# Kernel optimization log

Hardware: AMD Instinct MI355X
Metric: run time of the kernel (lower is better)

The kernel has to match this reference:

```python
import jax, jax.numpy as jnp
import numpy as np

B, T, D_MODEL = 2, 2048, 1024
EXPAND, D_STATE, D_CONV = 2, 16, 4
D_INNER = EXPAND * D_MODEL          # 2048
DT_RANK = (D_MODEL + 15) // 16      # 64 (mamba default: ceil(d_model/16))


def setup_inputs() -> dict:
    key = jax.random.key(0)
    ks = jax.random.split(key, 8)
    g = lambda k, shape, s: jax.random.normal(k, shape, dtype=jnp.float32) * s
    x = jax.random.normal(ks[0], (B, T, D_MODEL), dtype=jnp.float32)
    W_in = g(ks[1], (D_MODEL, 2 * D_INNER), 0.02)
    conv_w = g(ks[2], (D_INNER, D_CONV), 0.1)
    conv_b = jnp.zeros((D_INNER,), jnp.float32)
    W_xproj = g(ks[3], (D_INNER, DT_RANK + 2 * D_STATE), 0.02)
    W_dt = g(ks[4], (DT_RANK, D_INNER), 0.1)
    # dt bias so softplus(b_dt) ~ Uniform[1e-3, 0.1] (mamba init)
    dt = jnp.exp(jax.random.uniform(ks[5], (D_INNER,), jnp.float32)
                 * (np.log(0.1) - np.log(1e-3)) + np.log(1e-3))
    b_dt = dt + jnp.log(-jnp.expm1(-dt))  # inverse softplus
    # A_log init: log(1..d_state) broadcast over channels (S4D-real init)
    A_log = jnp.log(jnp.broadcast_to(
        jnp.arange(1, D_STATE + 1, dtype=jnp.float32), (D_INNER, D_STATE)))
    D = jnp.ones((D_INNER,), jnp.float32)
    W_out = g(ks[6], (D_INNER, D_MODEL), 0.02)
    return dict(x=x, W_in=W_in, conv_w=conv_w, conv_b=conv_b, W_xproj=W_xproj,
                W_dt=W_dt, b_dt=b_dt, A_log=A_log, D=D, W_out=W_out)


def _mamba(x, W_in, conv_w, conv_b, W_xproj, W_dt, b_dt, A_log, D, W_out):
    Bsz, Tlen, _ = x.shape
    xz = x @ W_in                                    # (B,T,2*d_inner)
    u, z = jnp.split(xz, 2, axis=-1)                 # each (B,T,d_inner)
    # causal depthwise conv1d (kernel D_CONV, left-padded)
    up = jnp.pad(u, ((0, 0), (D_CONV - 1, 0), (0, 0)))
    uc = conv_b + sum(up[:, k:k + Tlen, :] * conv_w[:, k] for k in range(D_CONV))
    uc = jax.nn.silu(uc)
    proj = uc @ W_xproj                              # (B,T,dt_rank+2N)
    dt, Bm, Cm = jnp.split(proj, [DT_RANK, DT_RANK + D_STATE], axis=-1)
    delta = jax.nn.softplus(dt @ W_dt + b_dt)        # (B,T,d_inner)
    A = -jnp.exp(A_log)                              # (d_inner,N)
    dA = jnp.exp(delta[..., None] * A)               # (B,T,d_inner,N)
    dBu = delta[..., None] * Bm[:, :, None, :] * uc[..., None]

    def step(h, inp):
        dA_t, dBu_t, C_t = inp                       # (B,d,N),(B,d,N),(B,N)
        h = dA_t * h + dBu_t
        y = jnp.einsum('bdn,bn->bd', h, C_t)
        return h, y

    h0 = jnp.zeros((Bsz, D_INNER, D_STATE), x.dtype)
    _, ys = jax.lax.scan(step, h0, (dA.transpose(1, 0, 2, 3),
                                    dBu.transpose(1, 0, 2, 3),
                                    Cm.transpose(1, 0, 2)))
    y = ys.transpose(1, 0, 2) + uc * D               # (B,T,d_inner)
    y = y * jax.nn.silu(z)                           # gate
    return y @ W_out                                 # (B,T,d_model)


def reference(x, W_in, conv_w, conv_b, W_xproj, W_dt, b_dt, A_log, D, W_out):
    return _mamba(x, W_in, conv_w, conv_b, W_xproj, W_dt, b_dt, A_log, D, W_out)
```

## Files before the change

kernel.cpp:

```cpp
#include <hip/hip_runtime.h>


#define NCHUNK 64
#define CLEN 32

typedef __attribute__((ext_vector_type(8))) short bf16x8;
typedef __attribute__((ext_vector_type(4))) float f32x4;

__device__ __forceinline__ float bf2f(ushort u) {
  union { unsigned u; float f; } x; x.u = ((unsigned)u) << 16; return x.f;
}
__device__ __forceinline__ ushort f2bf(float f) {
  union { float f; unsigned u; } x; x.f = f;
  unsigned r = x.u + 0x7FFFu + ((x.u >> 16) & 1u);
  return (ushort)(r >> 16);
}
__device__ __forceinline__ float siluf(float x) { return x / (1.f + __expf(-x)); }

__device__ __forceinline__ void pow_chain(float g, float* dA) {
  float e2 = g * g;
  float e4 = e2 * e2;
  float e8 = e4 * e4;
  dA[0] = g;        dA[1] = e2;       dA[2] = e2 * g;    dA[3] = e4;
  dA[4] = e4 * g;   dA[5] = e4 * e2;  dA[6] = e4 * dA[2]; dA[7] = e8;
  dA[8] = e8 * g;   dA[9] = e8 * e2;  dA[10] = e8 * dA[2]; dA[11] = e8 * e4;
  dA[12] = e8 * dA[4]; dA[13] = e8 * dA[5]; dA[14] = e8 * dA[6]; dA[15] = e8 * e8;
}

__device__ __forceinline__ void gl_lds16(const ushort* g, ushort* l) {
  __builtin_amdgcn_global_load_lds(
      (const __attribute__((address_space(1))) unsigned*)(size_t)g,
      (__attribute__((address_space(3))) unsigned*)(unsigned)(size_t)l,
      16, 0, 0);
}

__device__ __forceinline__ void phase_barrier() {
  __builtin_amdgcn_sched_barrier(0);
  __builtin_amdgcn_s_barrier();
  __builtin_amdgcn_sched_barrier(0);
}
#define VM8() asm volatile("s_waitcnt vmcnt(8)" ::: "memory")

__device__ __forceinline__ void transpose_tile(
    const float* __restrict__ src, ushort* __restrict__ dst, int K, int N,
    int kb, int nb, int tid, ushort (*tile)[33]) {
  const int tx = tid & 31, ty = tid >> 5;
  const int k0 = kb * 32, n0 = nb * 32;
#pragma unroll
  for (int i = 0; i < 4; ++i) {
    int k = k0 + ty + i * 8, n = n0 + tx;
    float v = (n < N) ? src[(size_t)k * N + n] : 0.f;
    tile[tx][ty + i * 8] = f2bf(v);
  }
  __syncthreads();
#pragma unroll
  for (int i = 0; i < 4; ++i) {
    int n = n0 + ty + i * 8, k = k0 + tx;
    dst[(size_t)n * K + k] = tile[ty + i * 8][tx];
  }
}

__global__ __launch_bounds__(256) void prep_kernel(
    const float* __restrict__ x, ushort* __restrict__ xb,
    const float* __restrict__ W_in, ushort* __restrict__ WibT,
    const float* __restrict__ W_xproj, ushort* __restrict__ WxbT,
    const float* __restrict__ W_dt, ushort* __restrict__ WdbT,
    const float* __restrict__ W_out, ushort* __restrict__ WobT) {
  __shared__ ushort tile[32][33];
  const int blk = blockIdx.x;
  const int tid = threadIdx.x;
  if (blk < 4096) {
    const int i = blk * 256 + tid;
    const float4 v = ((const float4*)x)[i];
    ushort4 o;
    o.x = f2bf(v.x); o.y = f2bf(v.y); o.z = f2bf(v.z); o.w = f2bf(v.w);
    ((ushort4*)xb)[i] = o;
  } else if (blk < 8192) {
    int t = blk - 4096;
    transpose_tile(W_in, WibT, 1024, 4096, t & 31, t >> 5, tid, tile);
  } else if (blk < 8448) {
    int t = blk - 8192;
    transpose_tile(W_xproj, WxbT, 2048, 96, t & 63, t >> 6, tid, tile);
  } else if (blk < 8576) {
    int t = blk - 8448;
    transpose_tile(W_dt, WdbT, 64, 2048, t & 1, t >> 1, tid, tile);
  } else {
    int t = blk - 8576;
    transpose_tile(W_out, WobT, 2048, 1024, t & 63, t >> 6, tid, tile);
  }
}

__device__ __forceinline__ void stage_half(
    const ushort* __restrict__ g, int rbase, int kbase, ushort* l,
    int wave, int lane, int Kfull) {
#pragma unroll
  for (int s2 = 0; s2 < 2; ++s2) {
    int slot = s2 * 512 + wave * 64 + lane;
    int row = slot >> 2;
    int kk = (slot & 3) ^ ((row >> 1) & 3);
    gl_lds16(g + (size_t)(rbase + row) * Kfull + kbase + kk * 8,
             l + (size_t)(s2 * 512 + wave * 64) * 8);
  }
}

__device__ __forceinline__ void rd_a(bf16x8* dst, const ushort* base,
                                     int wm, int lr, int sw8) {
#pragma unroll
  for (int mf = 0; mf < 8; ++mf)
    dst[mf] = *(const bf16x8*)&base[(wm * 128 + mf * 16 + lr) * 32 + sw8];
}
__device__ __forceinline__ void rd_b(bf16x8* dst, const ushort* base,
                                     int half, int wn, int lr, int sw8) {
  dst[0] = *(const bf16x8*)&base[(wn * 64 + half + lr) * 32 + sw8];
  dst[1] = *(const bf16x8*)&base[(wn * 64 + half + 16 + lr) * 32 + sw8];
}

template <int JB>
__device__ __forceinline__ void mfma_cluster(f32x4 (*acc)[4],
                                             const bf16x8* af,
                                             const bf16x8* bq) {
  __builtin_amdgcn_s_setprio(1);
#pragma unroll
  for (int mf = 0; mf < 8; ++mf)
#pragma unroll
    for (int n = 0; n < 2; ++n)
      acc[mf][JB + n] = __builtin_amdgcn_mfma_f32_16x16x32_bf16(
          af[mf], bq[n], acc[mf][JB + n], 0, 0, 0);
  __builtin_amdgcn_s_setprio(0);
}

template <int NT, int NB, int MODE>
__global__ __launch_bounds__(512, 2) void gemm256_kernel(
    const ushort* __restrict__ A, const ushort* __restrict__ Bt,
    void* __restrict__ Cv, int Kfull, int ldc, int zstride) {
  __shared__ alignas(16) ushort lds[2][4][8192];
  const int tid = threadIdx.x;
  const int wave = tid >> 6, lane = tid & 63;
  const int wm = wave >> 2, wn = wave & 3;
  const int lr = lane & 15, lq = lane >> 4;
  const int sw8 = (lq ^ ((lr >> 1) & 3)) * 8;
  const int s = ((blockIdx.x & 7) << 5) | (blockIdx.x >> 3);
  const int bm = (s & 15) << 8;
  const int r = s >> 4;
  const int bn = (r % NB) << 8;
  const int z = r / NB;
  const int kbeg = z * NT * 64;

  f32x4 acc[8][4];
#pragma unroll
  for (int i = 0; i < 8; ++i)
#pragma unroll
    for (int j = 0; j < 4; ++j) {
      f32x4 zz = {0.f, 0.f, 0.f, 0.f};
      acc[i][j] = zz;
    }
  bf16x8 af[8], b0[2], b1[2];

  ushort* l0 = &lds[0][0][0];
  ushort* l1 = &lds[1][0][0];

  stage_half(A,  bm, kbeg +  0, l0 +     0, wave, lane, Kfull);
  stage_half(Bt, bn, kbeg +  0, l0 + 16384, wave, lane, Kfull);
  stage_half(A,  bm, kbeg + 32, l0 +  8192, wave, lane, Kfull);
  stage_half(Bt, bn, kbeg + 32, l0 + 24576, wave, lane, Kfull);
  stage_half(A,  bm, kbeg + 64, l1 +     0, wave, lane, Kfull);
  stage_half(Bt, bn, kbeg + 64, l1 + 16384, wave, lane, Kfull);
  stage_half(A,  bm, kbeg + 96, l1 +  8192, wave, lane, Kfull);
  VM8();
  phase_barrier();
  rd_a(af, l0 + 0, wm, lr, sw8);
  rd_b(b0, l0 + 16384, 0, wn, lr, sw8);

  for (int t = 0; t < NT; ++t) {
    ushort* cur = (t & 1) ? l1 : l0;
    ushort* nxt = (t & 1) ? l0 : l1;
    const int k1c = kbeg + ((t + 1 < NT) ? (t + 1) : (NT - 1)) * 64;
    const int k2c = kbeg + ((t + 2 < NT) ? (t + 2) : (NT - 1)) * 64;

    rd_b(b1, cur + 16384, 32, wn, lr, sw8);
    stage_half(Bt, bn, k1c + 32, nxt + 24576, wave, lane, Kfull);
    mfma_cluster<0>(acc, af, b0);
    VM8();
    phase_barrier();

    rd_b(b0, cur + 24576, 0, wn, lr, sw8);
    stage_half(A, bm, k2c, cur + 0, wave, lane, Kfull);
    mfma_cluster<2>(acc, af, b1);
    rd_a(af, cur + 8192, wm, lr, sw8);
    VM8();
    phase_barrier();

    rd_b(b1, cur + 24576, 32, wn, lr, sw8);
    stage_half(Bt, bn, k2c, cur + 16384, wave, lane, Kfull);
    mfma_cluster<0>(acc, af, b0);
    VM8();
    phase_barrier();

    rd_b(b0, nxt + 16384, 0, wn, lr, sw8);
    stage_half(A, bm, k2c + 32, cur + 8192, wave, lane, Kfull);
    mfma_cluster<2>(acc, af, b1);
    rd_a(af, nxt + 0, wm, lr, sw8);
    VM8();
    phase_barrier();
  }

  if (MODE == 1) {
    ushort* C = (ushort*)Cv;
#pragma unroll
    for (int mf = 0; mf < 8; ++mf)
#pragma unroll
      for (int nf = 0; nf < 4; ++nf) {
        const int row0 = bm + wm * 128 + mf * 16 + lq * 4;
        const int col = bn + wn * 64 + nf * 16 + lr;
#pragma unroll
        for (int rr = 0; rr < 4; ++rr)
          C[(size_t)(row0 + rr) * ldc + col] = f2bf(acc[mf][nf][rr]);
      }
  } else {
    float* C = (float*)Cv + (size_t)z * zstride;
#pragma unroll
    for (int mf = 0; mf < 8; ++mf)
#pragma unroll
      for (int nf = 0; nf < 4; ++nf) {
        const int row0 = bm + wm * 128 + mf * 16 + lq * 4;
        const int col = bn + wn * 64 + nf * 16 + lr;
#pragma unroll
        for (int rr = 0; rr < 4; ++rr)
          C[(size_t)(row0 + rr) * ldc + col] = acc[mf][nf][rr];
      }
  }
}

template <int MODE>
__global__ __launch_bounds__(256) void gemm_tn_kernel(
    const ushort* __restrict__ A, const ushort* __restrict__ Bt,
    void* __restrict__ Cv, int N, int Kfull, int Kc, int ldc, int zstride) {
  __shared__ alignas(16) ushort smem[8192];
  ushort* As = smem;
  ushort* Bs = smem + 4096;
  const int tid = threadIdx.x;
  const int bm = blockIdx.x * 128;
  const int bn = blockIdx.y * 128;
  const int wave = tid >> 6, lane = tid & 63;
  const int wr = (wave >> 1) * 64, wc = (wave & 1) * 64;
  const int lr = lane & 15, lq = lane >> 4;
  const int sw8 = (lq ^ ((lr >> 1) & 3)) * 8;
  const int kbeg = blockIdx.z * Kc;

  f32x4 acc[4][4];
#pragma unroll
  for (int i = 0; i < 4; ++i)
#pragma unroll
    for (int j = 0; j < 4; ++j) {
      f32x4 z = {0.f, 0.f, 0.f, 0.f};
      acc[i][j] = z;
    }

  for (int k0 = kbeg; k0 < kbeg + Kc; k0 += 32) {
#pragma unroll
    for (int s = 0; s < 2; ++s) {
      int sb = s * 256 + wave * 64;
      int slot = sb + lane;
      int row = slot >> 2;
      int kk = (slot & 3) ^ ((row >> 1) & 3);
      gl_lds16(A + (size_t)(bm + row) * Kfull + k0 + kk * 8, &As[sb * 8]);
      gl_lds16(Bt + (size_t)(bn + row) * Kfull + k0 + kk * 8, &Bs[sb * 8]);
    }
    __syncthreads();

    bf16x8 af[4], bfr[4];
#pragma unroll
    for (int i = 0; i < 4; ++i)
      af[i] = *(const bf16x8*)&As[(wr + i * 16 + lr) * 32 + sw8];
#pragma unroll
    for (int j = 0; j < 4; ++j)
      bfr[j] = *(const bf16x8*)&Bs[(wc + j * 16 + lr) * 32 + sw8];
#pragma unroll
    for (int i = 0; i < 4; ++i)
#pragma unroll
      for (int j = 0; j < 4; ++j)
        acc[i][j] = __builtin_amdgcn_mfma_f32_16x16x32_bf16(af[i], bfr[j],
                                                            acc[i][j], 0, 0, 0);
    __syncthreads();
  }

  if (MODE == 0) {
#pragma unroll
    for (int i = 0; i < 4; ++i)
#pragma unroll
      for (int j = 0; j < 4; ++j) {
        int col = bn + wc + j * 16 + lr;
        if (col >= N) continue;
#pragma unroll
        for (int r = 0; r < 4; ++r) {
          int row = bm + wr + i * 16 + lq * 4 + r;
          ((float*)Cv)[(size_t)blockIdx.z * zstride + (size_t)row * ldc + col] =
              acc[i][j][r];
        }
      }
  }
}

__global__ __launch_bounds__(256) void gemm_delta_kernel(
    const ushort* __restrict__ A, const ushort* __restrict__ Bt,
    ushort* __restrict__ Cv, const float* __restrict__ bias) {
  __shared__ alignas(16) ushort As[128 * 32];
  __shared__ alignas(16) ushort Bs[128 * 32];
  const int tid = threadIdx.x;
  const int bm = blockIdx.x * 128;
  const int bn = blockIdx.y * 128;
  const int wave = tid >> 6, lane = tid & 63;
  const int wr = (wave >> 1) * 64, wc = (wave & 1) * 64;
  const int lr = lane & 15, lq = lane >> 4;
  const int sw8 = (lq ^ ((lr >> 1) & 3)) * 8;

  f32x4 acc[4][4];
#pragma unroll
  for (int i = 0; i < 4; ++i)
#pragma unroll
    for (int j = 0; j < 4; ++j) {
      f32x4 z = {0.f, 0.f, 0.f, 0.f};
      acc[i][j] = z;
    }

  for (int k0 = 0; k0 < 64; k0 += 32) {
#pragma unroll
    for (int s = 0; s < 2; ++s) {
      int sb = s * 256 + wave * 64;
      int slot = sb + lane;
      int row = slot >> 2;
      int kk = (slot & 3) ^ ((row >> 1) & 3);
      gl_lds16(A + (size_t)(bm + row) * 64 + k0 + kk * 8, &As[sb * 8]);
      gl_lds16(Bt + (size_t)(bn + row) * 64 + k0 + kk * 8, &Bs[sb * 8]);
    }
    __syncthreads();

    bf16x8 af[4], bfr[4];
#pragma unroll
    for (int i = 0; i < 4; ++i)
      af[i] = *(const bf16x8*)&As[(wr + i * 16 + lr) * 32 + sw8];
#pragma unroll
    for (int j = 0; j < 4; ++j)
      bfr[j] = *(const bf16x8*)&Bs[(wc + j * 16 + lr) * 32 + sw8];
#pragma unroll
    for (int i = 0; i < 4; ++i)
#pragma unroll
      for (int j = 0; j < 4; ++j)
        acc[i][j] = __builtin_amdgcn_mfma_f32_16x16x32_bf16(af[i], bfr[j],
                                                            acc[i][j], 0, 0, 0);
    __syncthreads();
  }

#pragma unroll
  for (int i = 0; i < 4; ++i)
#pragma unroll
    for (int j = 0; j < 4; ++j) {
      int col = bn + wc + j * 16 + lr;
      float bv = bias[col];
#pragma unroll
      for (int r = 0; r < 4; ++r) {
        int row = bm + wr + i * 16 + lq * 4 + r;
        float x = acc[i][j][r] + bv;
        float sp = (x > 20.f) ? x : __logf(1.f + __expf(x));
        Cv[(size_t)row * 2048 + col] = f2bf(sp);
      }
    }
}

__global__ __launch_bounds__(256) void reduce_proj_kernel(
    const float* __restrict__ part, float* __restrict__ proj,
    ushort* __restrict__ dtb) {
  const int idx = blockIdx.x * 256 + threadIdx.x;
  const int col = idx & 127;
  if (col >= 96) return;
  float s = 0.f;
#pragma unroll
  for (int z = 0; z < 8; ++z) s += part[(size_t)z * 524288 + idx];
  proj[idx] = s;
  if (col < 64) dtb[(size_t)(idx >> 7) * 64 + col] = f2bf(s);
}

__global__ __launch_bounds__(256) void reduce_out4_kernel(
    const float* __restrict__ p, float* __restrict__ out) {
  const int i = blockIdx.x * 256 + threadIdx.x;
  const float4* p4 = (const float4*)p;
  float4 a = p4[i];
  float4 b = p4[i + 1048576];
  float4 c = p4[i + 2097152];
  float4 d = p4[i + 3145728];
  float4 o = {a.x + b.x + c.x + d.x, a.y + b.y + c.y + d.y,
              a.z + b.z + c.z + d.z, a.w + b.w + c.w + d.w};
  ((float4*)out)[i] = o;
}

__global__ __launch_bounds__(256) void conv_silu_kernel(
    const ushort* __restrict__ xz, const float* __restrict__ conv_w,
    const float* __restrict__ conv_b, ushort* __restrict__ ucb) {
  const int idx = blockIdx.x * 256 + threadIdx.x;
  const int d4 = (idx & 511) * 4;
  const int bt = idx >> 9;
  const int t = bt & 2047;
  float4 acc = *(const float4*)(conv_b + d4);
  float4 w0 = *(const float4*)(conv_w + (d4 + 0) * 4);
  float4 w1 = *(const float4*)(conv_w + (d4 + 1) * 4);
  float4 w2 = *(const float4*)(conv_w + (d4 + 2) * 4);
  float4 w3 = *(const float4*)(conv_w + (d4 + 3) * 4);
  const float* wp[4] = {(const float*)&w0, (const float*)&w1,
                        (const float*)&w2, (const float*)&w3};
#pragma unroll
  for (int k = 0; k < 4; ++k) {
    int tt = t + k - 3;
    if (tt >= 0) {
      ushort4 v = *(const ushort4*)(xz + (size_t)(bt - t + tt) * 4096 + d4);
      acc.x += bf2f(v.x) * wp[0][k];
      acc.y += bf2f(v.y) * wp[1][k];
      acc.z += bf2f(v.z) * wp[2][k];
      acc.w += bf2f(v.w) * wp[3][k];
    }
  }
  ushort4 o;
  o.x = f2bf(siluf(acc.x)); o.y = f2bf(siluf(acc.y));
  o.z = f2bf(siluf(acc.z)); o.w = f2bf(siluf(acc.w));
  *(ushort4*)(ucb + (size_t)bt * 2048 + d4) = o;
}

__global__ __launch_bounds__(256) void scan_passA(
    const ushort* __restrict__ delta, const ushort* __restrict__ ucb,
    const float* __restrict__ proj, const float* __restrict__ A_log,
    float* __restrict__ hloc, float* __restrict__ Ssum) {
  __shared__ float Bsh[CLEN][16];
  const int tid = threadIdx.x;
  const int blk = blockIdx.x;
  const int dblk = blk & 7;
  const int c = (blk >> 3) & (NCHUNK - 1);
  const int b = blk >> 9;
  const int d = dblk * 256 + tid;
  const int t0 = c * CLEN;
  const size_t rowb = (size_t)b * 2048;

  const float a20 = -__expf(A_log[(size_t)d * 16]) * 1.44269504f;
#pragma unroll
  for (int s = 0; s < 2; ++s) {
    int e = s * 256 + tid;
    int tt = e >> 4, n = e & 15;
    Bsh[tt][n] = proj[(rowb + t0 + tt) * 128 + 64 + n];
  }
  __syncthreads();

  float h[16];
#pragma unroll
  for (int n = 0; n < 16; ++n) h[n] = 0.f;
  float S = 0.f;

  for (int tt = 0; tt < CLEN; ++tt) {
    size_t r = rowb + t0 + tt;
    float dlt = bf2f(delta[r * 2048 + d]);
    float u = bf2f(ucb[r * 2048 + d]);
    float du = dlt * u;
    S += dlt;
    float g = exp2f(dlt * a20);
    float dA[16];
    pow_chain(g, dA);
    const float* Bp = &Bsh[tt][0];
#pragma unroll
    for (int n = 0; n < 16; ++n) h[n] = dA[n] * h[n] + du * Bp[n];
  }
  float4* hp = (float4*)(hloc + ((size_t)(b * 2048 + d) * NCHUNK + c) * 16);
#pragma unroll
  for (int q = 0; q < 4; ++q) {
    float4 v = {h[q * 4], h[q * 4 + 1], h[q * 4 + 2], h[q * 4 + 3]};
    hp[q] = v;
  }
  Ssum[(size_t)(b * 2048 + d) * NCHUNK + c] = S;
}

__global__ __launch_bounds__(256) void scan_passB(
    float* __restrict__ hloc, const float* __restrict__ Ssum,
    const float* __restrict__ A_log) {
  const int gid = blockIdx.x * 256 + threadIdx.x;
  const int n = gid & 15;
  const int bd = gid >> 4;
  const int d = bd & 2047;
  const float a2 = -__expf(A_log[(size_t)d * 16 + n]) * 1.44269504f;
  float* hp = hloc + (size_t)bd * NCHUNK * 16 + n;
  const float* sp = Ssum + (size_t)bd * NCHUNK;
  float hs = 0.f;
#pragma unroll 8
  for (int c = 0; c < NCHUNK; ++c) {
    float v = hp[c * 16];
    float g = exp2f(a2 * sp[c]);
    hp[c * 16] = hs;
    hs = v + g * hs;
  }
}

__global__ __launch_bounds__(256) void scan_passC(
    const ushort* __restrict__ delta, const ushort* __restrict__ ucb,
    const float* __restrict__ proj, const ushort* __restrict__ xz,
    const float* __restrict__ A_log, const float* __restrict__ Dp,
    const float* __restrict__ hstart, ushort* __restrict__ yg) {
  __shared__ float Bsh[CLEN][16], Csh[CLEN][16];
  const int tid = threadIdx.x;
  const int blk = blockIdx.x;
  const int dblk = blk & 7;
  const int c = (blk >> 3) & (NCHUNK - 1);
  const int b = blk >> 9;
  const int d = dblk * 256 + tid;
  const int t0 = c * CLEN;
  const size_t rowb = (size_t)b * 2048;

  const float a20 = -__expf(A_log[(size_t)d * 16]) * 1.44269504f;
#pragma unroll
  for (int s = 0; s < 2; ++s) {
    int e = s * 256 + tid;
    int tt = e >> 4, n = e & 15;
    size_t r = rowb + t0 + tt;
    Bsh[tt][n] = proj[r * 128 + 64 + n];
    Csh[tt][n] = proj[r * 128 + 80 + n];
  }
  __syncthreads();

  float h[16];
  {
    const float4* hp =
        (const float4*)(hstart + ((size_t)(b * 2048 + d) * NCHUNK + c) * 16);
#pragma unroll
    for (int q = 0; q < 4; ++q) {
      float4 v = hp[q];
      h[q * 4 + 0] = v.x; h[q * 4 + 1] = v.y;
      h[q * 4 + 2] = v.z; h[q * 4 + 3] = v.w;
    }
  }
  const float Dd = Dp[d];

  for (int tt = 0; tt < CLEN; ++tt) {
    size_t r = rowb + t0 + tt;
    float dlt = bf2f(delta[r * 2048 + d]);
    float u = bf2f(ucb[r * 2048 + d]);
    float du = dlt * u;
    float g = exp2f(dlt * a20);
    float dA[16];
    pow_chain(g, dA);
    const float* Bp = &Bsh[tt][0];
    const float* Cp = &Csh[tt][0];
    float y0 = 0.f, y1 = 0.f, y2 = 0.f, y3 = 0.f;
#pragma unroll
    for (int n = 0; n < 16; n += 4) {
      h[n + 0] = dA[n + 0] * h[n + 0] + du * Bp[n + 0];
      h[n + 1] = dA[n + 1] * h[n + 1] + du * Bp[n + 1];
      h[n + 2] = dA[n + 2] * h[n + 2] + du * Bp[n + 2];
      h[n + 3] = dA[n + 3] * h[n + 3] + du * Bp[n + 3];
      y0 += h[n + 0] * Cp[n + 0];
      y1 += h[n + 1] * Cp[n + 1];
      y2 += h[n + 2] * Cp[n + 2];
      y3 += h[n + 3] * Cp[n + 3];
    }
    float y = (y0 + y1) + (y2 + y3);
    float yv = y + u * Dd;
    float zv = bf2f(xz[r * 4096 + 2048 + d]);
    yg[r * 2048 + d] = f2bf(yv * siluf(zv));
  }
}

extern "C" void kernel_launch(void* const* d_in, const int* in_sizes, int n_in,
                              void* d_out, int out_size, void* d_ws,
                              size_t ws_size, hipStream_t stream) {
  const float* x       = (const float*)d_in[0];
  const float* W_in    = (const float*)d_in[1];
  const float* conv_w  = (const float*)d_in[2];
  const float* conv_b  = (const float*)d_in[3];
  const float* W_xproj = (const float*)d_in[4];
  const float* W_dt    = (const float*)d_in[5];
  const float* b_dt    = (const float*)d_in[6];
  const float* A_log   = (const float*)d_in[7];
  const float* Dp      = (const float*)d_in[8];
  const float* W_out   = (const float*)d_in[9];

  char* ws = (char*)d_ws;
  ushort* xb    = (ushort*)(ws);
  ushort* WibT  = (ushort*)(ws + 8388608);
  ushort* WxbT  = (ushort*)(ws + 16777216);
  ushort* WdbT  = (ushort*)(ws + 17301504);
  ushort* WobT  = (ushort*)(ws + 17563648);
  ushort* xz    = (ushort*)(ws + 21757952);
  ushort* ucb   = (ushort*)(ws + 55312384);
  float*  proj  = (float*)(ws + 72089600);
  ushort* dtb   = (ushort*)(ws + 74186752);
  ushort* delta = (ushort*)(ws + 74711040);
  ushort* yg    = (ushort*)(ws + 91488256);
  float*  hloc  = (float*)(ws + 108265472);
  float*  Ssum  = (float*)(ws + 125042688);
  float*  part  = (float*)(ws + 126091264);
  float*  opart = (float*)(ws + 21757952);

  prep_kernel<<<10624, 256, 0, stream>>>(x, xb, W_in, WibT, W_xproj, WxbT,
                                         W_dt, WdbT, W_out, WobT);
  gemm256_kernel<16, 16, 1><<<256, 512, 0, stream>>>(
      xb, WibT, xz, 1024, 4096, 0);
  conv_silu_kernel<<<8192, 256, 0, stream>>>(xz, conv_w, conv_b, ucb);
  gemm_tn_kernel<0><<<dim3(32, 1, 8), 256, 0, stream>>>(
      ucb, WxbT, part, 96, 2048, 256, 128, 524288);
  reduce_proj_kernel<<<2048, 256, 0, stream>>>(part, proj, dtb);
  gemm_delta_kernel<<<dim3(32, 16), 256, 0, stream>>>(dtb, WdbT, delta, b_dt);
  scan_passA<<<1024, 256, 0, stream>>>(delta, ucb, proj, A_log, hloc, Ssum);
  scan_passB<<<256, 256, 0, stream>>>(hloc, Ssum, A_log);
  scan_passC<<<1024, 256, 0, stream>>>(delta, ucb, proj, xz, A_log, Dp, hloc,
                                       yg);
  gemm256_kernel<8, 4, 0><<<256, 512, 0, stream>>>(
      yg, WobT, opart, 2048, 1024, 4194304);
  reduce_out4_kernel<<<4096, 256, 0, stream>>>(opart, (float*)d_out);
}
```

Measured before the change: 298.9 us.

## Fuse conv into proj GEMM, fold split-K reductions, atomic output accumulation

The depthwise conv+SiLU is computed inside the x_proj GEMM's A-tile load, which also writes ucb, so the separate conv kernel goes away. The proj split-K partial sum is folded into the delta GEMM's A-operand staging and into the scan kernels' B/C loads. The out-projection split-K now accumulates with atomic adds into a zeroed output instead of a separate reduce kernel. This saves launches and intermediate memory traffic, at the cost of redundant partial reads in the scans, nondeterministic fp32 atomic ordering, and conv work repeated across the 8 split-K blocks... actually each z slice handles distinct channels.

```diff
diff --git a/kernel.cpp b/kernel.cpp
--- a/kernel.cpp
+++ b/kernel.cpp
@@ -65,7 +65,8 @@
     const float* __restrict__ W_in, ushort* __restrict__ WibT,
     const float* __restrict__ W_xproj, ushort* __restrict__ WxbT,
     const float* __restrict__ W_dt, ushort* __restrict__ WdbT,
-    const float* __restrict__ W_out, ushort* __restrict__ WobT) {
+    const float* __restrict__ W_out, ushort* __restrict__ WobT,
+    float* __restrict__ dout) {
   __shared__ ushort tile[32][33];
   const int blk = blockIdx.x;
   const int tid = threadIdx.x;
@@ -84,9 +85,13 @@
   } else if (blk < 8576) {
     int t = blk - 8448;
     transpose_tile(W_dt, WdbT, 64, 2048, t & 1, t >> 1, tid, tile);
-  } else {
+  } else if (blk < 10624) {
     int t = blk - 8576;
     transpose_tile(W_out, WobT, 2048, 1024, t & 63, t >> 6, tid, tile);
+  } else {
+    const int i = (blk - 10624) * 256 + tid;
+    float4 zz = {0.f, 0.f, 0.f, 0.f};
+    ((float4*)dout)[i] = zz;
   }
 }
 
@@ -132,7 +137,7 @@
 template <int NT, int NB, int MODE>
 __global__ __launch_bounds__(512, 2) void gemm256_kernel(
     const ushort* __restrict__ A, const ushort* __restrict__ Bt,
-    void* __restrict__ Cv, int Kfull, int ldc, int zstride) {
+    void* __restrict__ Cv, int Kfull, int ldc) {
   __shared__ alignas(16) ushort lds[2][4][8192];
   const int tid = threadIdx.x;
   const int wave = tid >> 6, lane = tid & 63;
@@ -217,7 +222,7 @@
           C[(size_t)(row0 + rr) * ldc + col] = f2bf(acc[mf][nf][rr]);
       }
   } else {
-    float* C = (float*)Cv + (size_t)z * zstride;
+    float* C = (float*)Cv;
 #pragma unroll
     for (int mf = 0; mf < 8; ++mf)
 #pragma unroll
@@ -226,18 +231,118 @@
         const int col = bn + wn * 64 + nf * 16 + lr;
 #pragma unroll
         for (int rr = 0; rr < 4; ++rr)
-          C[(size_t)(row0 + rr) * ldc + col] = acc[mf][nf][rr];
+          unsafeAtomicAdd(&C[(size_t)(row0 + rr) * ldc + col],
+                          acc[mf][nf][rr]);
       }
   }
 }
 
-template <int MODE>
-__global__ __launch_bounds__(256) void gemm_tn_kernel(
-    const ushort* __restrict__ A, const ushort* __restrict__ Bt,
-    void* __restrict__ Cv, int N, int Kfull, int Kc, int ldc, int zstride) {
-  __shared__ alignas(16) ushort smem[8192];
-  ushort* As = smem;
-  ushort* Bs = smem + 4096;
+__global__ __launch_bounds__(256) void gemm_proj_kernel(
+    const ushort* __restrict__ xz, const ushort* __restrict__ Bt,
+    const float* __restrict__ conv_w, const float* __restrict__ conv_b,
+    ushort* __restrict__ ucb, float* __restrict__ part) {
+  __shared__ alignas(16) ushort As[4096];
+  __shared__ alignas(16) ushort Bs[4096];
+  const int tid = threadIdx.x;
+  const int bm = blockIdx.x * 128;
+  const int z = blockIdx.y;
+  const int kbeg = z * 256;
+  const int wave = tid >> 6, lane = tid & 63;
+  const int wr = (wave >> 1) * 64, wc = (wave & 1) * 64;
+  const int lr = lane & 15, lq = lane >> 4;
+  const int sw8 = (lq ^ ((lr >> 1) & 3)) * 8;
+
+  f32x4 acc[4][4];
+#pragma unroll
+  for (int i = 0; i < 4; ++i)
+#pragma unroll
+    for (int j = 0; j < 4; ++j) {
+      f32x4 zz = {0.f, 0.f, 0.f, 0.f};
+      acc[i][j] = zz;
+    }
+
+  for (int k0 = 0; k0 < 256; k0 += 32) {
+#pragma unroll
+    for (int qq = 0; qq < 2; ++qq) {
+      const int q = tid * 2 + qq;
+      const int row_l = q >> 2, kc = q & 3;
+      const int row_g = bm + row_l;
+      const int t = row_g & 2047;
+      const int dg = kbeg + k0 + kc * 8;
+      float v[8];
+      {
+        float4 cb0 = *(const float4*)(conv_b + dg);
+        float4 cb1 = *(const float4*)(conv_b + dg + 4);
+        v[0] = cb0.x; v[1] = cb0.y; v[2] = cb0.z; v[3] = cb0.w;
+        v[4] = cb1.x; v[5] = cb1.y; v[6] = cb1.z; v[7] = cb1.w;
+      }
+      float4 w[8];
+#pragma unroll
+      for (int e = 0; e < 8; ++e)
+        w[e] = *(const float4*)(conv_w + (dg + e) * 4);
+#pragma unroll
+      for (int k = 0; k < 4; ++k) {
+        int tt = t + k - 3;
+        if (tt >= 0) {
+          bf16x8 xv =
+              *(const bf16x8*)(xz + (size_t)(row_g + k - 3) * 4096 + dg);
+#pragma unroll
+          for (int e = 0; e < 8; ++e)
+            v[e] += bf2f((ushort)xv[e]) * ((const float*)&w[e])[k];
+        }
+      }
+      bf16x8 o;
+#pragma unroll
+      for (int e = 0; e < 8; ++e) o[e] = (short)f2bf(siluf(v[e]));
+      *(bf16x8*)(ucb + (size_t)row_g * 2048 + dg) = o;
+      const int c = kc ^ ((row_l >> 1) & 3);
+      *(bf16x8*)&As[row_l * 32 + c * 8] = o;
+    }
+#pragma unroll
+    for (int s2 = 0; s2 < 2; ++s2) {
+      int sb = s2 * 256 + wave * 64;
+      int slot = sb + lane;
+      int row = slot >> 2;
+      int kk = (slot & 3) ^ ((row >> 1) & 3);
+      gl_lds16(Bt + (size_t)row * 2048 + kbeg + k0 + kk * 8, &Bs[sb * 8]);
+    }
+    __syncthreads();
+
+    bf16x8 af[4], bfr[4];
+#pragma unroll
+    for (int i = 0; i < 4; ++i)
+      af[i] = *(const bf16x8*)&As[(wr + i * 16 + lr) * 32 + sw8];
+#pragma unroll
+    for (int j = 0; j < 4; ++j)
+      bfr[j] = *(const bf16x8*)&Bs[(wc + j * 16 + lr) * 32 + sw8];
+#pragma unroll
+    for (int i = 0; i < 4; ++i)
+#pragma unroll
+      for (int j = 0; j < 4; ++j)
+        acc[i][j] = __builtin_amdgcn_mfma_f32_16x16x32_bf16(af[i], bfr[j],
+                                                            acc[i][j], 0, 0, 0);
+    __syncthreads();
+  }
+
+#pragma unroll
+  for (int i = 0; i < 4; ++i)
+#pragma unroll
+    for (int j = 0; j < 4; ++j) {
+      int col = wc + j * 16 + lr;
+      if (col >= 96) continue;
+#pragma unroll
+      for (int r = 0; r < 4; ++r) {
+        int row = bm + wr + i * 16 + lq * 4 + r;
+        part[(size_t)z * 524288 + (size_t)row * 128 + col] = acc[i][j][r];
+      }
+    }
+}
+
+__global__ __launch_bounds__(256) void gemm_delta_kernel(
+    const float* __restrict__ part, const ushort* __restrict__ Bt,
+    ushort* __restrict__ Cv, const float* __restrict__ bias) {
+  __shared__ alignas(16) ushort As[2][4096];
+  __shared__ alignas(16) ushort Bs[4096];
   const int tid = threadIdx.x;
   const int bm = blockIdx.x * 128;
   const int bn = blockIdx.y * 128;
@@ -245,100 +350,54 @@
   const int wr = (wave >> 1) * 64, wc = (wave & 1) * 64;
   const int lr = lane & 15, lq = lane >> 4;
   const int sw8 = (lq ^ ((lr >> 1) & 3)) * 8;
-  const int kbeg = blockIdx.z * Kc;
 
   f32x4 acc[4][4];
 #pragma unroll
   for (int i = 0; i < 4; ++i)
 #pragma unroll
     for (int j = 0; j < 4; ++j) {
-      f32x4 z = {0.f, 0.f, 0.f, 0.f};
-      acc[i][j] = z;
-    }
-
-  for (int k0 = kbeg; k0 < kbeg + Kc; k0 += 32) {
-#pragma unroll
-    for (int s = 0; s < 2; ++s) {
-      int sb = s * 256 + wave * 64;
+      f32x4 zz = {0.f, 0.f, 0.f, 0.f};
+      acc[i][j] = zz;
+    }
+
+#pragma unroll
+  for (int qq = 0; qq < 4; ++qq) {
+    const int q = tid * 4 + qq;
+    const int row_l = q >> 3, kc6 = q & 7;
+    const int slab = kc6 >> 2, kcs = kc6 & 3;
+    const float* p = part + (size_t)(bm + row_l) * 128 + kc6 * 8;
+    float v[8];
+#pragma unroll
+    for (int e = 0; e < 8; ++e) v[e] = 0.f;
+#pragma unroll
+    for (int z = 0; z < 8; ++z) {
+      float4 a = *(const float4*)(p + (size_t)z * 524288);
+      float4 b = *(const float4*)(p + (size_t)z * 524288 + 4);
+      v[0] += a.x; v[1] += a.y; v[2] += a.z; v[3] += a.w;
+      v[4] += b.x; v[5] += b.y; v[6] += b.z; v[7] += b.w;
+    }
+    bf16x8 o;
+#pragma unroll
+    for (int e = 0; e < 8; ++e) o[e] = (short)f2bf(v[e]);
+    const int c = kcs ^ ((row_l >> 1) & 3);
+    *(bf16x8*)&As[slab][row_l * 32 + c * 8] = o;
+  }
+
+  for (int s = 0; s < 2; ++s) {
+#pragma unroll
+    for (int s2 = 0; s2 < 2; ++s2) {
+      int sb = s2 * 256 + wave * 64;
       int slot = sb + lane;
       int row = slot >> 2;
       int kk = (slot & 3) ^ ((row >> 1) & 3);
-      gl_lds16(A + (size_t)(bm + row) * Kfull + k0 + kk * 8, &As[sb * 8]);
-      gl_lds16(Bt + (size_t)(bn + row) * Kfull + k0 + kk * 8, &Bs[sb * 8]);
+      gl_lds16(Bt + (size_t)(bn + row) * 64 + s * 32 + kk * 8, &Bs[sb * 8]);
     }
     __syncthreads();
 
     bf16x8 af[4], bfr[4];
 #pragma unroll
     for (int i = 0; i < 4; ++i)
-      af[i] = *(const bf16x8*)&As[(wr + i * 16 + lr) * 32 + sw8];
-#pragma unroll
-    for (int j = 0; j < 4; ++j)
-      bfr[j] = *(const bf16x8*)&Bs[(wc + j * 16 + lr) * 32 + sw8];
-#pragma unroll
-    for (int i = 0; i < 4; ++i)
-#pragma unroll
-      for (int j = 0; j < 4; ++j)
-        acc[i][j] = __builtin_amdgcn_mfma_f32_16x16x32_bf16(af[i], bfr[j],
-                                                            acc[i][j], 0, 0, 0);
-    __syncthreads();
-  }
-
-  if (MODE == 0) {
-#pragma unroll
-    for (int i = 0; i < 4; ++i)
-#pragma unroll
-      for (int j = 0; j < 4; ++j) {
-        int col = bn + wc + j * 16 + lr;
-        if (col >= N) continue;
-#pragma unroll
-        for (int r = 0; r < 4; ++r) {
-          int row = bm + wr + i * 16 + lq * 4 + r;
-          ((float*)Cv)[(size_t)blockIdx.z * zstride + (size_t)row * ldc + col] =
-              acc[i][j][r];
-        }
-      }
-  }
-}
-
-__global__ __launch_bounds__(256) void gemm_delta_kernel(
-    const ushort* __restrict__ A, const ushort* __restrict__ Bt,
-    ushort* __restrict__ Cv, const float* __restrict__ bias) {
-  __shared__ alignas(16) ushort As[128 * 32];
-  __shared__ alignas(16) ushort Bs[128 * 32];
-  const int tid = threadIdx.x;
-  const int bm = blockIdx.x * 128;
-  const int bn = blockIdx.y * 128;
-  const int wave = tid >> 6, lane = tid & 63;
-  const int wr = (wave >> 1) * 64, wc = (wave & 1) * 64;
-  const int lr = lane & 15, lq = lane >> 4;
-  const int sw8 = (lq ^ ((lr >> 1) & 3)) * 8;
-
-  f32x4 acc[4][4];
-#pragma unroll
-  for (int i = 0; i < 4; ++i)
-#pragma unroll
-    for (int j = 0; j < 4; ++j) {
-      f32x4 z = {0.f, 0.f, 0.f, 0.f};
-      acc[i][j] = z;
-    }
-
-  for (int k0 = 0; k0 < 64; k0 += 32) {
-#pragma unroll
-    for (int s = 0; s < 2; ++s) {
-      int sb = s * 256 + wave * 64;
-      int slot = sb + lane;
-      int row = slot >> 2;
-      int kk = (slot & 3) ^ ((row >> 1) & 3);
-      gl_lds16(A + (size_t)(bm + row) * 64 + k0 + kk * 8, &As[sb * 8]);
-      gl_lds16(Bt + (size_t)(bn + row) * 64 + k0 + kk * 8, &Bs[sb * 8]);
-    }
-    __syncthreads();
-
-    bf16x8 af[4], bfr[4];
-#pragma unroll
-    for (int i = 0; i < 4; ++i)
-      af[i] = *(const bf16x8*)&As[(wr + i * 16 + lr) * 32 + sw8];
+      af[i] = *(const bf16x8*)&As[s][(wr + i * 16 + lr) * 32 + sw8];
 #pragma unroll
     for (int j = 0; j < 4; ++j)
       bfr[j] = *(const bf16x8*)&Bs[(wc + j * 16 + lr) * 32 + sw8];
@@ -367,66 +426,9 @@
     }
 }
 
-__global__ __launch_bounds__(256) void reduce_proj_kernel(
-    const float* __restrict__ part, float* __restrict__ proj,
-    ushort* __restrict__ dtb) {
-  const int idx = blockIdx.x * 256 + threadIdx.x;
-  const int col = idx & 127;
-  if (col >= 96) return;
-  float s = 0.f;
-#pragma unroll
-  for (int z = 0; z < 8; ++z) s += part[(size_t)z * 524288 + idx];
-  proj[idx] = s;
-  if (col < 64) dtb[(size_t)(idx >> 7) * 64 + col] = f2bf(s);
-}
-
-__global__ __launch_bounds__(256) void reduce_out4_kernel(
-    const float* __restrict__ p, float* __restrict__ out) {
-  const int i = blockIdx.x * 256 + threadIdx.x;
-  const float4* p4 = (const float4*)p;
-  float4 a = p4[i];
-  float4 b = p4[i + 1048576];
-  float4 c = p4[i + 2097152];
-  float4 d = p4[i + 3145728];
-  float4 o = {a.x + b.x + c.x + d.x, a.y + b.y + c.y + d.y,
-              a.z + b.z + c.z + d.z, a.w + b.w + c.w + d.w};
-  ((float4*)out)[i] = o;
-}
-
-__global__ __launch_bounds__(256) void conv_silu_kernel(
-    const ushort* __restrict__ xz, const float* __restrict__ conv_w,
-    const float* __restrict__ conv_b, ushort* __restrict__ ucb) {
-  const int idx = blockIdx.x * 256 + threadIdx.x;
-  const int d4 = (idx & 511) * 4;
-  const int bt = idx >> 9;
-  const int t = bt & 2047;
-  float4 acc = *(const float4*)(conv_b + d4);
-  float4 w0 = *(const float4*)(conv_w + (d4 + 0) * 4);
-  float4 w1 = *(const float4*)(conv_w + (d4 + 1) * 4);
-  float4 w2 = *(const float4*)(conv_w + (d4 + 2) * 4);
-  float4 w3 = *(const float4*)(conv_w + (d4 + 3) * 4);
-  const float* wp[4] = {(const float*)&w0, (const float*)&w1,
-                        (const float*)&w2, (const float*)&w3};
-#pragma unroll
-  for (int k = 0; k < 4; ++k) {
-    int tt = t + k - 3;
-    if (tt >= 0) {
-      ushort4 v = *(const ushort4*)(xz + (size_t)(bt - t + tt) * 4096 + d4);
-      acc.x += bf2f(v.x) * wp[0][k];
-      acc.y += bf2f(v.y) * wp[1][k];
-      acc.z += bf2f(v.z) * wp[2][k];
-      acc.w += bf2f(v.w) * wp[3][k];
-    }
-  }
-  ushort4 o;
-  o.x = f2bf(siluf(acc.x)); o.y = f2bf(siluf(acc.y));
-  o.z = f2bf(siluf(acc.z)); o.w = f2bf(siluf(acc.w));
-  *(ushort4*)(ucb + (size_t)bt * 2048 + d4) = o;
-}
-
 __global__ __launch_bounds__(256) void scan_passA(
     const ushort* __restrict__ delta, const ushort* __restrict__ ucb,
-    const float* __restrict__ proj, const float* __restrict__ A_log,
+    const float* __restrict__ part, const float* __restrict__ A_log,
     float* __restrict__ hloc, float* __restrict__ Ssum) {
   __shared__ float Bsh[CLEN][16];
   const int tid = threadIdx.x;
@@ -443,7 +445,11 @@
   for (int s = 0; s < 2; ++s) {
     int e = s * 256 + tid;
     int tt = e >> 4, n = e & 15;
-    Bsh[tt][n] = proj[(rowb + t0 + tt) * 128 + 64 + n];
+    size_t base = (rowb + t0 + tt) * 128 + 64 + n;
+    float acc = 0.f;
+#pragma unroll
+    for (int z = 0; z < 8; ++z) acc += part[base + (size_t)z * 524288];
+    Bsh[tt][n] = acc;
   }
   __syncthreads();
 
@@ -496,7 +502,7 @@
 
 __global__ __launch_bounds__(256) void scan_passC(
     const ushort* __restrict__ delta, const ushort* __restrict__ ucb,
-    const float* __restrict__ proj, const ushort* __restrict__ xz,
+    const float* __restrict__ part, const ushort* __restrict__ xz,
     const float* __restrict__ A_log, const float* __restrict__ Dp,
     const float* __restrict__ hstart, ushort* __restrict__ yg) {
   __shared__ float Bsh[CLEN][16], Csh[CLEN][16];
@@ -514,9 +520,15 @@
   for (int s = 0; s < 2; ++s) {
     int e = s * 256 + tid;
     int tt = e >> 4, n = e & 15;
-    size_t r = rowb + t0 + tt;
-    Bsh[tt][n] = proj[r * 128 + 64 + n];
-    Csh[tt][n] = proj[r * 128 + 80 + n];
+    size_t base = (rowb + t0 + tt) * 128 + n;
+    float accB = 0.f, accC = 0.f;
+#pragma unroll
+    for (int z = 0; z < 8; ++z) {
+      accB += part[base + 64 + (size_t)z * 524288];
+      accC += part[base + 80 + (size_t)z * 524288];
+    }
+    Bsh[tt][n] = accB;
+    Csh[tt][n] = accC;
   }
   __syncthreads();
 
@@ -584,29 +596,22 @@
   ushort* WobT  = (ushort*)(ws + 17563648);
   ushort* xz    = (ushort*)(ws + 21757952);
   ushort* ucb   = (ushort*)(ws + 55312384);
-  float*  proj  = (float*)(ws + 72089600);
-  ushort* dtb   = (ushort*)(ws + 74186752);
   ushort* delta = (ushort*)(ws + 74711040);
   ushort* yg    = (ushort*)(ws + 91488256);
   float*  hloc  = (float*)(ws + 108265472);
   float*  Ssum  = (float*)(ws + 125042688);
   float*  part  = (float*)(ws + 126091264);
-  float*  opart = (float*)(ws + 21757952);
-
-  prep_kernel<<<10624, 256, 0, stream>>>(x, xb, W_in, WibT, W_xproj, WxbT,
-                                         W_dt, WdbT, W_out, WobT);
-  gemm256_kernel<16, 16, 1><<<256, 512, 0, stream>>>(
-      xb, WibT, xz, 1024, 4096, 0);
-  conv_silu_kernel<<<8192, 256, 0, stream>>>(xz, conv_w, conv_b, ucb);
-  gemm_tn_kernel<0><<<dim3(32, 1, 8), 256, 0, stream>>>(
-      ucb, WxbT, part, 96, 2048, 256, 128, 524288);
-  reduce_proj_kernel<<<2048, 256, 0, stream>>>(part, proj, dtb);
-  gemm_delta_kernel<<<dim3(32, 16), 256, 0, stream>>>(dtb, WdbT, delta, b_dt);
-  scan_passA<<<1024, 256, 0, stream>>>(delta, ucb, proj, A_log, hloc, Ssum);
+
+  prep_kernel<<<14720, 256, 0, stream>>>(x, xb, W_in, WibT, W_xproj, WxbT,
+                                         W_dt, WdbT, W_out, WobT,
+                                         (float*)d_out);
+  gemm256_kernel<16, 16, 1><<<256, 512, 0, stream>>>(xb, WibT, xz, 1024, 4096);
+  gemm_proj_kernel<<<dim3(32, 8), 256, 0, stream>>>(xz, WxbT, conv_w, conv_b,
+                                                    ucb, part);
+  gemm_delta_kernel<<<dim3(32, 16), 256, 0, stream>>>(part, WdbT, delta, b_dt);
+  scan_passA<<<1024, 256, 0, stream>>>(delta, ucb, part, A_log, hloc, Ssum);
   scan_passB<<<256, 256, 0, stream>>>(hloc, Ssum, A_log);
-  scan_passC<<<1024, 256, 0, stream>>>(delta, ucb, proj, xz, A_log, Dp, hloc,
+  scan_passC<<<1024, 256, 0, stream>>>(delta, ucb, part, xz, A_log, Dp, hloc,
                                        yg);
-  gemm256_kernel<8, 4, 0><<<256, 512, 0, stream>>>(
-      yg, WobT, opart, 2048, 1024, 4194304);
-  reduce_out4_kernel<<<4096, 256, 0, stream>>>(opart, (float*)d_out);
-}
+  gemm256_kernel<8, 4, 2><<<256, 512, 0, stream>>>(yg, WobT, d_out, 2048, 1024);
+}
```

New measurement: 344.8 us. 15.4% more time.

## Fuse three scan passes into one cooperative kernel with grid syncs

Applied to the files above, without the earlier changes.

Merges the chunked scan's three kernels (local chunk scan, inter-chunk carry propagation, final output pass) into one cooperative kernel that separates the phases with grid-wide barriers. This removes two kernel launches and their gaps, and keeps the B/C chunk data in shared memory across phases. In exchange, all 1024 blocks must be co-resident, and the carry phase runs on only 256 blocks while the rest wait at the barrier. The template parameter on the tn GEMM is also dropped as cleanup.

```diff
diff --git a/kernel.cpp b/kernel.cpp
--- a/kernel.cpp
+++ b/kernel.cpp
@@ -1,4 +1,7 @@
 #include <hip/hip_runtime.h>
+#include <hip/hip_cooperative_groups.h>
+
+namespace cg = cooperative_groups;
 
 
 #define NCHUNK 64
@@ -231,10 +234,9 @@
   }
 }
 
-template <int MODE>
 __global__ __launch_bounds__(256) void gemm_tn_kernel(
     const ushort* __restrict__ A, const ushort* __restrict__ Bt,
-    void* __restrict__ Cv, int N, int Kfull, int Kc, int ldc, int zstride) {
+    float* __restrict__ Cv, int N, int Kfull, int Kc, int ldc, int zstride) {
   __shared__ alignas(16) ushort smem[8192];
   ushort* As = smem;
   ushort* Bs = smem + 4096;
@@ -284,21 +286,19 @@
     __syncthreads();
   }
 
-  if (MODE == 0) {
-#pragma unroll
-    for (int i = 0; i < 4; ++i)
-#pragma unroll
-      for (int j = 0; j < 4; ++j) {
-        int col = bn + wc + j * 16 + lr;
-        if (col >= N) continue;
-#pragma unroll
-        for (int r = 0; r < 4; ++r) {
-          int row = bm + wr + i * 16 + lq * 4 + r;
-          ((float*)Cv)[(size_t)blockIdx.z * zstride + (size_t)row * ldc + col] =
-              acc[i][j][r];
-        }
+#pragma unroll
+  for (int i = 0; i < 4; ++i)
+#pragma unroll
+    for (int j = 0; j < 4; ++j) {
+      int col = bn + wc + j * 16 + lr;
+      if (col >= N) continue;
+#pragma unroll
+      for (int r = 0; r < 4; ++r) {
+        int row = bm + wr + i * 16 + lq * 4 + r;
+        Cv[(size_t)blockIdx.z * zstride + (size_t)row * ldc + col] =
+            acc[i][j][r];
       }
-  }
+    }
 }
 
 __global__ __launch_bounds__(256) void gemm_delta_kernel(
@@ -424,81 +424,13 @@
   *(ushort4*)(ucb + (size_t)bt * 2048 + d4) = o;
 }
 
-__global__ __launch_bounds__(256) void scan_passA(
-    const ushort* __restrict__ delta, const ushort* __restrict__ ucb,
-    const float* __restrict__ proj, const float* __restrict__ A_log,
-    float* __restrict__ hloc, float* __restrict__ Ssum) {
-  __shared__ float Bsh[CLEN][16];
-  const int tid = threadIdx.x;
-  const int blk = blockIdx.x;
-  const int dblk = blk & 7;
-  const int c = (blk >> 3) & (NCHUNK - 1);
-  const int b = blk >> 9;
-  const int d = dblk * 256 + tid;
-  const int t0 = c * CLEN;
-  const size_t rowb = (size_t)b * 2048;
-
-  const float a20 = -__expf(A_log[(size_t)d * 16]) * 1.44269504f;
-#pragma unroll
-  for (int s = 0; s < 2; ++s) {
-    int e = s * 256 + tid;
-    int tt = e >> 4, n = e & 15;
-    Bsh[tt][n] = proj[(rowb + t0 + tt) * 128 + 64 + n];
-  }
-  __syncthreads();
-
-  float h[16];
-#pragma unroll
-  for (int n = 0; n < 16; ++n) h[n] = 0.f;
-  float S = 0.f;
-
-  for (int tt = 0; tt < CLEN; ++tt) {
-    size_t r = rowb + t0 + tt;
-    float dlt = bf2f(delta[r * 2048 + d]);
-    float u = bf2f(ucb[r * 2048 + d]);
-    float du = dlt * u;
-    S += dlt;
-    float g = exp2f(dlt * a20);
-    float dA[16];
-    pow_chain(g, dA);
-    const float* Bp = &Bsh[tt][0];
-#pragma unroll
-    for (int n = 0; n < 16; ++n) h[n] = dA[n] * h[n] + du * Bp[n];
-  }
-  float4* hp = (float4*)(hloc + ((size_t)(b * 2048 + d) * NCHUNK + c) * 16);
-#pragma unroll
-  for (int q = 0; q < 4; ++q) {
-    float4 v = {h[q * 4], h[q * 4 + 1], h[q * 4 + 2], h[q * 4 + 3]};
-    hp[q] = v;
-  }
-  Ssum[(size_t)(b * 2048 + d) * NCHUNK + c] = S;
-}
-
-__global__ __launch_bounds__(256) void scan_passB(
-    float* __restrict__ hloc, const float* __restrict__ Ssum,
-    const float* __restrict__ A_log) {
-  const int gid = blockIdx.x * 256 + threadIdx.x;
-  const int n = gid & 15;
-  const int bd = gid >> 4;
-  const int d = bd & 2047;
-  const float a2 = -__expf(A_log[(size_t)d * 16 + n]) * 1.44269504f;
-  float* hp = hloc + (size_t)bd * NCHUNK * 16 + n;
-  const float* sp = Ssum + (size_t)bd * NCHUNK;
-  float hs = 0.f;
-#pragma unroll 8
-  for (int c = 0; c < NCHUNK; ++c) {
-    float v = hp[c * 16];
-    float g = exp2f(a2 * sp[c]);
-    hp[c * 16] = hs;
-    hs = v + g * hs;
-  }
-}
-
-__global__ __launch_bounds__(256) void scan_passC(
+__global__ __launch_bounds__(256) void scan_fused_kernel(
     const ushort* __restrict__ delta, const ushort* __restrict__ ucb,
     const float* __restrict__ proj, const ushort* __restrict__ xz,
     const float* __restrict__ A_log, const float* __restrict__ Dp,
-    const float* __restrict__ hstart, ushort* __restrict__ yg) {
+    float* __restrict__ hloc, float* __restrict__ Ssum,
+    ushort* __restrict__ yg) {
+  cg::grid_group grid = cg::this_grid();
   __shared__ float Bsh[CLEN][16], Csh[CLEN][16];
   const int tid = threadIdx.x;
   const int blk = blockIdx.x;
@@ -520,45 +452,94 @@
   }
   __syncthreads();
 
-  float h[16];
   {
+    float h[16];
+#pragma unroll
+    for (int n = 0; n < 16; ++n) h[n] = 0.f;
+    float S = 0.f;
+    for (int tt = 0; tt < CLEN; ++tt) {
+      size_t r = rowb + t0 + tt;
+      float dlt = bf2f(delta[r * 2048 + d]);
+      float u = bf2f(ucb[r * 2048 + d]);
+      float du = dlt * u;
+      S += dlt;
+      float g = exp2f(dlt * a20);
+      float dA[16];
+      pow_chain(g, dA);
+      const float* Bp = &Bsh[tt][0];
+#pragma unroll
+      for (int n = 0; n < 16; ++n) h[n] = dA[n] * h[n] + du * Bp[n];
+    }
+    float4* hp = (float4*)(hloc + ((size_t)(b * 2048 + d) * NCHUNK + c) * 16);
+#pragma unroll
+    for (int q = 0; q < 4; ++q) {
+      float4 v = {h[q * 4], h[q * 4 + 1], h[q * 4 + 2], h[q * 4 + 3]};
+      hp[q] = v;
+    }
+    Ssum[(size_t)(b * 2048 + d) * NCHUNK + c] = S;
+  }
+  __threadfence();
+  grid.sync();
+
+  if (blk < 256) {
+    const int gid = blk * 256 + tid;
+    const int n = gid & 15;
+    const int bd = gid >> 4;
+    const int dd = bd & 2047;
+    const float a2 = -__expf(A_log[(size_t)dd * 16 + n]) * 1.44269504f;
+    float* hp = hloc + (size_t)bd * NCHUNK * 16 + n;
+    const float* sp = Ssum + (size_t)bd * NCHUNK;
+    float hs = 0.f;
+#pragma unroll 8
+    for (int cc = 0; cc < NCHUNK; ++cc) {
+      float v = hp[cc * 16];
+      float g = exp2f(a2 * sp[cc]);
+      hp[cc * 16] = hs;
+      hs = v + g * hs;
+    }
+  }
+  __threadfence();
+  grid.sync();
+
+  {
+    float h[16];
     const float4* hp =
-        (const float4*)(hstart + ((size_t)(b * 2048 + d) * NCHUNK + c) * 16);
+        (const float4*)(hloc + ((size_t)(b * 2048 + d) * NCHUNK + c) * 16);
 #pragma unroll
     for (int q = 0; q < 4; ++q) {
       float4 v = hp[q];
       h[q * 4 + 0] = v.x; h[q * 4 + 1] = v.y;
       h[q * 4 + 2] = v.z; h[q * 4 + 3] = v.w;
     }
-  }
-  const float Dd = Dp[d];
-
-  for (int tt = 0; tt < CLEN; ++tt) {
-    size_t r = rowb + t0 + tt;
-    float dlt = bf2f(delta[r * 2048 + d]);
-    float u = bf2f(ucb[r * 2048 + d]);
-    float du = dlt * u;
-    float g = exp2f(dlt * a20);
-    float dA[16];
-    pow_chain(g, dA);
-    const float* Bp = &Bsh[tt][0];
-    const float* Cp = &Csh[tt][0];
-    float y0 = 0.f, y1 = 0.f, y2 = 0.f, y3 = 0.f;
-#pragma unroll
-    for (int n = 0; n < 16; n += 4) {
-      h[n + 0] = dA[n + 0] * h[n + 0] + du * Bp[n + 0];
-      h[n + 1] = dA[n + 1] * h[n + 1] + du * Bp[n + 1];
-      h[n + 2] = dA[n + 2] * h[n + 2] + du * Bp[n + 2];
-      h[n + 3] = dA[n + 3] * h[n + 3] + du * Bp[n + 3];
-      y0 += h[n + 0] * Cp[n + 0];
-      y1 += h[n + 1] * Cp[n + 1];
-      y2 += h[n + 2] * Cp[n + 2];
-      y3 += h[n + 3] * Cp[n + 3];
-    }
-    float y = (y0 + y1) + (y2 + y3);
-    float yv = y + u * Dd;
-    float zv = bf2f(xz[r * 4096 + 2048 + d]);
-    yg[r * 2048 + d] = f2bf(yv * siluf(zv));
+    const float Dd = Dp[d];
+
+    for (int tt = 0; tt < CLEN; ++tt) {
+      size_t r = rowb + t0 + tt;
+      float dlt = bf2f(delta[r * 2048 + d]);
+      float u = bf2f(ucb[r * 2048 + d]);
+      float du = dlt * u;
+      float g = exp2f(dlt * a20);
+      float dA[16];
+      pow_chain(g, dA);
+      const float* Bp = &Bsh[tt][0];
+      const float* Cp = &Csh[tt][0];
+      float y0 = 0.f, y1 = 0.f, y2 = 0.f, y3 = 0.f;
+#pragma unroll
+      for (int n = 0; n < 16; n += 4) {
+        h[n + 0] = dA[n + 0] * h[n + 0] + du * Bp[n + 0];
+        h[n + 1] = dA[n + 1] * h[n + 1] + du * Bp[n + 1];
+        h[n + 2] = dA[n + 2] * h[n + 2] + du * Bp[n + 2];
+        h[n + 3] = dA[n + 3] * h[n + 3] + du * Bp[n + 3];
+        y0 += h[n + 0] * Cp[n + 0];
+        y1 += h[n + 1] * Cp[n + 1];
+        y2 += h[n + 2] * Cp[n + 2];
+        y3 += h[n + 3] * Cp[n + 3];
+      }
+      float y = (y0 + y1) + (y2 + y3);
+      float yv = y + u * Dd;
+      float zv = bf2f(xz[r * 4096 + 2048 + d]);
+      yg[r * 2048 + d] = f2bf(yv * siluf(zv));
+    }
   }
 }
 
@@ -598,14 +579,17 @@
   gemm256_kernel<16, 16, 1><<<256, 512, 0, stream>>>(
       xb, WibT, xz, 1024, 4096, 0);
   conv_silu_kernel<<<8192, 256, 0, stream>>>(xz, conv_w, conv_b, ucb);
-  gemm_tn_kernel<0><<<dim3(32, 1, 8), 256, 0, stream>>>(
+  gemm_tn_kernel<<<dim3(32, 1, 8), 256, 0, stream>>>(
       ucb, WxbT, part, 96, 2048, 256, 128, 524288);
   reduce_proj_kernel<<<2048, 256, 0, stream>>>(part, proj, dtb);
   gemm_delta_kernel<<<dim3(32, 16), 256, 0, stream>>>(dtb, WdbT, delta, b_dt);
-  scan_passA<<<1024, 256, 0, stream>>>(delta, ucb, proj, A_log, hloc, Ssum);
-  scan_passB<<<256, 256, 0, stream>>>(hloc, Ssum, A_log);
-  scan_passC<<<1024, 256, 0, stream>>>(delta, ucb, proj, xz, A_log, Dp, hloc,
-                                       yg);
+  {
+    void* args[] = {(void*)&delta, (void*)&ucb, (void*)&proj, (void*)&xz,
+                    (void*)&A_log, (void*)&Dp, (void*)&hloc, (void*)&Ssum,
+                    (void*)&yg};
+    hipLaunchCooperativeKernel((void*)scan_fused_kernel, dim3(1024), dim3(256),
+                               args, 0, stream);
+  }
   gemm256_kernel<8, 4, 0><<<256, 512, 0, stream>>>(
       yg, WobT, opart, 2048, 1024, 4194304);
   reduce_out4_kernel<<<4096, 256, 0, stream>>>(opart, (float*)d_out);
```

Result: slower. 752.3 us (+151.7%).
